# Performance work log

Measured on AMD Instinct MI355X. Metric: run time of the kernel, lower is better.

Reference implementation:

```python
import jax, jax.numpy as jnp
import numpy as np

KNN_K = 200
NUM_CLASSES = 400
TEMPERATURE = 0.07


def setup_inputs() -> dict:
    key = jax.random.key(0)
    k1, k2, k3 = jax.random.split(key, 3)
    q_knn = jax.random.normal(k1, (256, 128), dtype=jnp.float32)
    memory = jax.random.normal(k2, (500000, 128), dtype=jnp.float32)
    train_labels = jax.random.randint(k3, (500000,), 0, NUM_CLASSES, dtype=jnp.int64)
    return {"q_knn": q_knn, "memory": memory, "train_labels": train_labels}


def reference(q_knn, memory, train_labels):
    # dist: [N, M] similarity matmul (einsum 'nc,mc->nm')
    dist = jnp.einsum("nc,mc->nm", q_knn, memory)
    # top-k neighbors (sorted, largest)
    yd, yi = jax.lax.top_k(dist, KNN_K)          # [N, K], [N, K]
    retrieval = train_labels[yi]                  # [N, K] gathered labels
    # weighted one-hot vote: scatter-add exp(yd / T) into class bins
    w = jnp.exp(yd / TEMPERATURE)                 # [N, K]
    n = q_knn.shape[0]
    rows = jnp.arange(n)[:, None]                 # [N, 1] broadcast over K
    preds = jnp.zeros((n, NUM_CLASSES), dtype=q_knn.dtype).at[rows, retrieval].add(w)
    return preds
```

## Files before the change

### kernel.cpp

```cpp
#include <hip/hip_runtime.h>
#include <cfloat>
#include <math.h>


#define N_Q 256
#define KDIM 128
#define M_MEM 500000
#define NUM_CLASSES 400
#define KNN_K 200
#define INV_T (1.0f / 0.07f)
#define EXP_ARG_CLAMP 80.0f
#define Z_THR 3.0f

#define CAP_MAX 8192
#define PADB 136
#define M_TILE 64
#define T_PER 11
#define N_TILES64 7813
#define GEMM_GRID 711
#define BUF_CAP 1024

#define OFF_THR 0
#define OFF_CNT 1024
#define OFF_FLAG 2048
#define OFF_AFRAG 4096
#define OFF_CAND 69632

typedef __attribute__((ext_vector_type(8))) short short8;
typedef __attribute__((ext_vector_type(4))) float f32x4;

__device__ __forceinline__ unsigned short f2bf(float x) {
    unsigned u = __float_as_uint(x);
    return (unsigned short)((u + 0x7fffu + ((u >> 16) & 1u)) >> 16);
}

__global__ __launch_bounds__(256) void k_prep(const float* __restrict__ q,
                                              float* __restrict__ thr,
                                              int* __restrict__ cnt,
                                              int* __restrict__ flag,
                                              const int* __restrict__ lab32,
                                              short* __restrict__ afrag) {
    int tid = threadIdx.x;
    if (blockIdx.x == 0) {
        const float4* q4 = (const float4*)q;
        float s = 0.f;
#pragma unroll 8
        for (int i = 0; i < 32; i++) {
            float4 v = q4[tid * 32 + i];
            s = fmaf(v.x, v.x, s);
            s = fmaf(v.y, v.y, s);
            s = fmaf(v.z, v.z, s);
            s = fmaf(v.w, v.w, s);
        }
        thr[tid] = Z_THR * sqrtf(s);
        cnt[tid] = 0;
        __shared__ int s_any;
        if (tid == 0) s_any = 0;
        __syncthreads();
        int any = 0;
        for (int i = tid; i < 1024; i += 256) any |= lab32[2 * i + 1];
        if (any) atomicOr(&s_any, 1);
        __syncthreads();
        if (tid == 0) *flag = (s_any == 0) ? 1 : 0;
    } else {
        int e = (blockIdx.x - 1) * 256 + tid;
        int lane = e & 63, ks = (e >> 6) & 3, NT = e >> 8;
        int n = NT * 16 + (lane & 15);
        int k0 = ks * 32 + (lane >> 4) * 8;
        const float4* q4 = (const float4*)q;
        float4 a = q4[n * 32 + k0 / 4];
        float4 b = q4[n * 32 + k0 / 4 + 1];
        short8 o;
        o[0] = f2bf(a.x); o[1] = f2bf(a.y); o[2] = f2bf(a.z); o[3] = f2bf(a.w);
        o[4] = f2bf(b.x); o[5] = f2bf(b.y); o[6] = f2bf(b.z); o[7] = f2bf(b.w);
        ((short8*)afrag)[e] = o;
    }
}

#define PF_ISSUE(PF, TILE)                                                   \
    {                                                                        \
        int mb_ = m0 + (TILE) * M_TILE;                                      \
        _Pragma("unroll") for (int p = 0; p < 4; p++) {                      \
            int gm = mb_ + p * 16 + row0;                                    \
            if (gm >= M_MEM) gm = M_MEM - 1;                                 \
            int gi = gm * 32 + kg * 2;                                       \
            PF[p][0] = mem4[gi];                                             \
            PF[p][1] = mem4[gi + 1];                                         \
        }                                                                    \
    }

#define TILE_BODY(T, PF, BUFIDX)                                             \
    {                                                                        \
        short* B = Bs[BUFIDX];                                               \
        _Pragma("unroll") for (int p = 0; p < 4; p++) {                      \
            short8 o;                                                        \
            o[0] = f2bf(PF[p][0].x); o[1] = f2bf(PF[p][0].y);                \
            o[2] = f2bf(PF[p][0].z); o[3] = f2bf(PF[p][0].w);                \
            o[4] = f2bf(PF[p][1].x); o[5] = f2bf(PF[p][1].y);                \
            o[6] = f2bf(PF[p][1].z); o[7] = f2bf(PF[p][1].w);                \
            *(short8*)&B[(p * 16 + row0) * PADB + kg * 8] = o;               \
        }                                                                    \
        __syncthreads();                                                     \
        if ((T) + 2 < ntile) PF_ISSUE(PF, (T) + 2);                          \
        int mt0 = m0 + (T) * M_TILE;                                         \
        _Pragma("unroll") for (int mt = 0; mt < 4; mt++) {                   \
            int mrow = mt * 16 + ml;                                         \
            short8 bf[4];                                                    \
            _Pragma("unroll") for (int ks = 0; ks < 4; ks++)                 \
                bf[ks] = *(const short8*)&B[mrow * PADB + ks * 32 + quad * 8];\
            f32x4 acc[4];                                                    \
            _Pragma("unroll") for (int nt = 0; nt < 4; nt++)                 \
                acc[nt] = (f32x4){0.f, 0.f, 0.f, 0.f};                       \
            _Pragma("unroll") for (int nt = 0; nt < 4; nt++)                 \
                _Pragma("unroll") for (int ks = 0; ks < 4; ks++)             \
                    acc[nt] = __builtin_amdgcn_mfma_f32_16x16x32_bf16(       \
                        af[nt][ks], bf[ks], acc[nt], 0, 0, 0);               \
            int m = mt0 + mt * 16 + ml;                                      \
            bool mvalid = (m < M_MEM);                                       \
            _Pragma("unroll") for (int nt = 0; nt < 4; nt++) {               \
                bool any = (acc[nt][0] >= tr[nt][0]) |                       \
                           (acc[nt][1] >= tr[nt][1]) |                       \
                           (acc[nt][2] >= tr[nt][2]) |                       \
                           (acc[nt][3] >= tr[nt][3]);                        \
                if (mvalid & any) {                                          \
                    int nb = wn + nt * 16 + quad * 4;                        \
                    _Pragma("unroll") for (int r = 0; r < 4; r++) {          \
                        float v = acc[nt][r];                                \
                        if (v >= tr[nt][r]) {                                \
                            int p = atomicAdd(&s_nap, 1);                    \
                            if (p < BUF_CAP)                                 \
                                sbuf[p] = make_uint2(                        \
                                    __float_as_uint(v),                      \
                                    (unsigned)m | ((unsigned)(nb + r) << 19));\
                        }                                                    \
                    }                                                        \
                }                                                            \
            }                                                                \
        }                                                                    \
    }

__global__ __launch_bounds__(256) void k_gemm(const short* __restrict__ afrag,
                                              const float* __restrict__ mem,
                                              const float* __restrict__ thr,
                                              int* __restrict__ cnt,
                                              uint2* __restrict__ cand,
                                              int cap) {
    __shared__ short Bs[2][M_TILE * PADB];
    __shared__ uint2 sbuf[BUF_CAP];
    __shared__ int s_nap;
    int tid = threadIdx.x, lane = tid & 63, w = tid >> 6;
    int quad = lane >> 4, ml = lane & 15;
    int wn = w * 64;

    if (tid == 0) s_nap = 0;

    short8 af[4][4];
    const short8* afv = (const short8*)afrag;
#pragma unroll
    for (int nt = 0; nt < 4; nt++) {
        int NT = w * 4 + nt;
#pragma unroll
        for (int ks = 0; ks < 4; ks++) af[nt][ks] = afv[(NT * 4 + ks) * 64 + lane];
    }
    float tr[4][4];
#pragma unroll
    for (int nt = 0; nt < 4; nt++)
#pragma unroll
        for (int r = 0; r < 4; r++) tr[nt][r] = thr[wn + nt * 16 + quad * 4 + r];

    int t0 = blockIdx.x * T_PER;
    int ntile = N_TILES64 - t0;
    if (ntile > T_PER) ntile = T_PER;

    int row0 = tid >> 4, kg = tid & 15;
    const float4* mem4 = (const float4*)mem;
    int m0 = t0 * M_TILE;

    float4 pfA[4][2], pfB[4][2];
    if (ntile > 0) PF_ISSUE(pfA, 0);
    if (ntile > 1) PF_ISSUE(pfB, 1);

    for (int t = 0; t < ntile; t += 2) {
        TILE_BODY(t, pfA, 0);
        if (t + 1 < ntile) TILE_BODY(t + 1, pfB, 1);
    }

    __syncthreads();
    int total = s_nap;
    if (total > BUF_CAP) total = BUF_CAP;
    for (int i = tid; i < total; i += 256) {
        uint2 e = sbuf[i];
        int n = (int)(e.y >> 19);
        unsigned m = e.y & 0x7FFFFu;
        int pos = atomicAdd(&cnt[n], 1);
        if (pos < cap) cand[(long)n * cap + pos] = make_uint2(e.x, m);
    }
}

__global__ __launch_bounds__(256) void k_select(const uint2* __restrict__ cand,
                                                const int* __restrict__ cnt,
                                                const int* __restrict__ lab32,
                                                const int* __restrict__ flag,
                                                float* __restrict__ out, int cap) {
    __shared__ float sv[CAP_MAX];
    __shared__ float bins[NUM_CLASSES];
    int r = blockIdx.x, tid = threadIdx.x;
    int is64 = *flag;
    int cn = cnt[r];
    if (cn > cap) cn = cap;
    for (int i = tid; i < NUM_CLASSES; i += 256) bins[i] = 0.f;
    const uint2* cr = &cand[(long)r * cap];
    for (int i = tid; i < cn; i += 256) sv[i] = __uint_as_float(cr[i].x);
    __syncthreads();

    float v0 = -FLT_MAX, v1 = -FLT_MAX, v2 = -FLT_MAX, v3 = -FLT_MAX;
    if (tid < cn)       v0 = sv[tid];
    if (tid + 256 < cn) v1 = sv[tid + 256];
    if (tid + 512 < cn) v2 = sv[tid + 512];
    if (tid + 768 < cn) v3 = sv[tid + 768];
    int r0 = 0, r1 = 0, r2 = 0, r3 = 0;
    for (int i = 0; i < cn; i++) {
        float x = sv[i];
        r0 += (x > v0);
        r1 += (x > v1);
        r2 += (x > v2);
        r3 += (x > v3);
    }
#define VOTE(c, val, rk, valid)                                              \
    if ((valid) && (rk) < KNN_K) {                                           \
        int mm = (int)cr[c].y;                                               \
        int lab = is64 ? lab32[2 * mm] : lab32[mm];                          \
        if ((unsigned)lab < NUM_CLASSES) {                                   \
                \
            float wgt = expf(fminf((val) * INV_T, EXP_ARG_CLAMP));           \
            atomicAdd(&bins[lab], wgt);                                      \
        }                                                                    \
    }
    VOTE(tid, v0, r0, tid < cn)
    VOTE(tid + 256, v1, r1, tid + 256 < cn)
    VOTE(tid + 512, v2, r2, tid + 512 < cn)
    VOTE(tid + 768, v3, r3, tid + 768 < cn)
#undef VOTE
    __syncthreads();
    for (int c = tid; c < NUM_CLASSES; c += 256)
        out[r * NUM_CLASSES + c] = bins[c];
}

extern "C" void kernel_launch(void* const* d_in, const int* in_sizes, int n_in,
                              void* d_out, int out_size, void* d_ws, size_t ws_size,
                              hipStream_t stream) {
    const float* q = (const float*)d_in[0];
    const float* mem = (const float*)d_in[1];
    const int* lab = (const int*)d_in[2];
    float* out = (float*)d_out;

    char* ws = (char*)d_ws;
    float* thr = (float*)(ws + OFF_THR);
    int* cnt = (int*)(ws + OFF_CNT);
    int* flag = (int*)(ws + OFF_FLAG);
    short* afrag = (short*)(ws + OFF_AFRAG);
    uint2* cand = (uint2*)(ws + OFF_CAND);

    int cap = CAP_MAX;
    if (ws_size > OFF_CAND) {
        size_t maxcap = (ws_size - OFF_CAND) / (256ull * 8ull);
        if ((size_t)cap > maxcap) cap = (int)maxcap;
    }

    k_prep<<<17, 256, 0, stream>>>(q, thr, cnt, flag, lab, afrag);
    k_gemm<<<GEMM_GRID, 256, 0, stream>>>(afrag, mem, thr, cnt, cand, cap);
    k_select<<<256, 256, 0, stream>>>(cand, cnt, lab, flag, out, cap);
}
```

Baseline: 439.1 us.

## Restructure GEMM so each wave owns memory rows and streams all queries from LDS

Swaps the roles in the similarity GEMM. Query fragments and thresholds now sit in LDS, and each wave loads its own 16 memory rows straight from global memory into registers as the B operand, covering all 256 queries with 16 accumulator tiles. This drops the shared B staging buffer and the per-tile __syncthreads, and the grid becomes 512 blocks of 4 waves striding over 31250 row groups. In exchange every MFMA now reads its A operand from LDS, and holding 64 accumulator registers per thread may lower occupancy.

```diff
diff --git a/kernel.cpp b/kernel.cpp
--- a/kernel.cpp
+++ b/kernel.cpp
@@ -13,11 +13,9 @@
 #define Z_THR 3.0f
 
 #define CAP_MAX 8192
-#define PADB 136
-#define M_TILE 64
-#define T_PER 11
-#define N_TILES64 7813
-#define GEMM_GRID 711
+#define NBODY 31250
+#define NWAVES 2048
+#define GEMM_GRID 512
 #define BUF_CAP 1024
 
 #define OFF_THR 0
@@ -77,62 +75,54 @@
     }
 }
 
-#define PF_ISSUE(PF, TILE)                                                   \
+#define PF_ISSUE(BANK, S)                                                    \
     {                                                                        \
-        int mb_ = m0 + (TILE) * M_TILE;                                      \
-        _Pragma("unroll") for (int p = 0; p < 4; p++) {                      \
-            int gm = mb_ + p * 16 + row0;                                    \
-            if (gm >= M_MEM) gm = M_MEM - 1;                                 \
-            int gi = gm * 32 + kg * 2;                                       \
-            PF[p][0] = mem4[gi];                                             \
-            PF[p][1] = mem4[gi + 1];                                         \
-        }                                                                    \
-    }
-
-#define TILE_BODY(T, PF, BUFIDX)                                             \
+        int fi_ = ((g + (S) * NWAVES) * 16 + ml) * 32 + quad * 2;            \
+        _Pragma("unroll") for (int ks = 0; ks < 4; ks++) {                   \
+            BANK[ks * 2]     = mem4[fi_ + ks * 8];                           \
+            BANK[ks * 2 + 1] = mem4[fi_ + ks * 8 + 1];                       \
+        }                                                                    \
+    }
+
+#define BODY(S, BANK)                                                        \
     {                                                                        \
-        short* B = Bs[BUFIDX];                                               \
-        _Pragma("unroll") for (int p = 0; p < 4; p++) {                      \
+        short8 bf[4];                                                        \
+        _Pragma("unroll") for (int ks = 0; ks < 4; ks++) {                   \
             short8 o;                                                        \
-            o[0] = f2bf(PF[p][0].x); o[1] = f2bf(PF[p][0].y);                \
-            o[2] = f2bf(PF[p][0].z); o[3] = f2bf(PF[p][0].w);                \
-            o[4] = f2bf(PF[p][1].x); o[5] = f2bf(PF[p][1].y);                \
-            o[6] = f2bf(PF[p][1].z); o[7] = f2bf(PF[p][1].w);                \
-            *(short8*)&B[(p * 16 + row0) * PADB + kg * 8] = o;               \
-        }                                                                    \
-        __syncthreads();                                                     \
-        if ((T) + 2 < ntile) PF_ISSUE(PF, (T) + 2);                          \
-        int mt0 = m0 + (T) * M_TILE;                                         \
-        _Pragma("unroll") for (int mt = 0; mt < 4; mt++) {                   \
-            int mrow = mt * 16 + ml;                                         \
-            short8 bf[4];                                                    \
-            _Pragma("unroll") for (int ks = 0; ks < 4; ks++)                 \
-                bf[ks] = *(const short8*)&B[mrow * PADB + ks * 32 + quad * 8];\
-            f32x4 acc[4];                                                    \
-            _Pragma("unroll") for (int nt = 0; nt < 4; nt++)                 \
-                acc[nt] = (f32x4){0.f, 0.f, 0.f, 0.f};                       \
-            _Pragma("unroll") for (int nt = 0; nt < 4; nt++)                 \
-                _Pragma("unroll") for (int ks = 0; ks < 4; ks++)             \
-                    acc[nt] = __builtin_amdgcn_mfma_f32_16x16x32_bf16(       \
-                        af[nt][ks], bf[ks], acc[nt], 0, 0, 0);               \
-            int m = mt0 + mt * 16 + ml;                                      \
-            bool mvalid = (m < M_MEM);                                       \
-            _Pragma("unroll") for (int nt = 0; nt < 4; nt++) {               \
-                bool any = (acc[nt][0] >= tr[nt][0]) |                       \
-                           (acc[nt][1] >= tr[nt][1]) |                       \
-                           (acc[nt][2] >= tr[nt][2]) |                       \
-                           (acc[nt][3] >= tr[nt][3]);                        \
-                if (mvalid & any) {                                          \
-                    int nb = wn + nt * 16 + quad * 4;                        \
-                    _Pragma("unroll") for (int r = 0; r < 4; r++) {          \
-                        float v = acc[nt][r];                                \
-                        if (v >= tr[nt][r]) {                                \
-                            int p = atomicAdd(&s_nap, 1);                    \
-                            if (p < BUF_CAP)                                 \
-                                sbuf[p] = make_uint2(                        \
-                                    __float_as_uint(v),                      \
-                                    (unsigned)m | ((unsigned)(nb + r) << 19));\
-                        }                                                    \
+            o[0] = f2bf(BANK[ks * 2].x);     o[1] = f2bf(BANK[ks * 2].y);    \
+            o[2] = f2bf(BANK[ks * 2].z);     o[3] = f2bf(BANK[ks * 2].w);    \
+            o[4] = f2bf(BANK[ks * 2 + 1].x); o[5] = f2bf(BANK[ks * 2 + 1].y);\
+            o[6] = f2bf(BANK[ks * 2 + 1].z); o[7] = f2bf(BANK[ks * 2 + 1].w);\
+            bf[ks] = o;                                                      \
+        }                                                                    \
+        if ((S) + 2 < nb) PF_ISSUE(BANK, (S) + 2);                           \
+        f32x4 acc[16];                                                       \
+        _Pragma("unroll") for (int nt = 0; nt < 16; nt++)                    \
+            acc[nt] = (f32x4){0.f, 0.f, 0.f, 0.f};                           \
+        _Pragma("unroll") for (int nt = 0; nt < 16; nt++)                    \
+            _Pragma("unroll") for (int ks = 0; ks < 4; ks++) {               \
+                short8 a8 = af_lds[(nt * 4 + ks) * 64 + lane];               \
+                acc[nt] = __builtin_amdgcn_mfma_f32_16x16x32_bf16(           \
+                    a8, bf[ks], acc[nt], 0, 0, 0);                           \
+            }                                                                \
+        int m = (g + (S) * NWAVES) * 16 + ml;                                \
+        _Pragma("unroll") for (int nt = 0; nt < 16; nt++) {                  \
+            float4 tv = *(const float4*)&thr_lds[nt * 16 + quad * 4];        \
+            bool any = (acc[nt][0] >= tv.x) | (acc[nt][1] >= tv.y) |         \
+                       (acc[nt][2] >= tv.z) | (acc[nt][3] >= tv.w);          \
+            if (any) {                                                       \
+                int nb_ = nt * 16 + quad * 4;                                \
+                float tr0 = tv.x, tr1 = tv.y, tr2 = tv.z, tr3 = tv.w;        \
+                _Pragma("unroll") for (int r = 0; r < 4; r++) {              \
+                    float v = acc[nt][r];                                    \
+                    float trr = (r == 0) ? tr0 : (r == 1) ? tr1              \
+                              : (r == 2) ? tr2 : tr3;                        \
+                    if (v >= trr) {                                          \
+                        int p = atomicAdd(&s_nap, 1);                        \
+                        if (p < BUF_CAP)                                     \
+                            sbuf[p] = make_uint2(                            \
+                                __float_as_uint(v),                          \
+                                (unsigned)m | ((unsigned)(nb_ + r) << 19));  \
                     }                                                        \
                 }                                                            \
             }                                                                \
@@ -145,44 +135,31 @@
                                               int* __restrict__ cnt,
                                               uint2* __restrict__ cand,
                                               int cap) {
-    __shared__ short Bs[2][M_TILE * PADB];
+    __shared__ short8 af_lds[4096];
+    __shared__ float thr_lds[256];
     __shared__ uint2 sbuf[BUF_CAP];
     __shared__ int s_nap;
     int tid = threadIdx.x, lane = tid & 63, w = tid >> 6;
     int quad = lane >> 4, ml = lane & 15;
-    int wn = w * 64;
 
     if (tid == 0) s_nap = 0;
-
-    short8 af[4][4];
     const short8* afv = (const short8*)afrag;
 #pragma unroll
-    for (int nt = 0; nt < 4; nt++) {
-        int NT = w * 4 + nt;
-#pragma unroll
-        for (int ks = 0; ks < 4; ks++) af[nt][ks] = afv[(NT * 4 + ks) * 64 + lane];
-    }
-    float tr[4][4];
-#pragma unroll
-    for (int nt = 0; nt < 4; nt++)
-#pragma unroll
-        for (int r = 0; r < 4; r++) tr[nt][r] = thr[wn + nt * 16 + quad * 4 + r];
-
-    int t0 = blockIdx.x * T_PER;
-    int ntile = N_TILES64 - t0;
-    if (ntile > T_PER) ntile = T_PER;
-
-    int row0 = tid >> 4, kg = tid & 15;
+    for (int i = 0; i < 16; i++) af_lds[i * 256 + tid] = afv[i * 256 + tid];
+    thr_lds[tid] = thr[tid];
+    __syncthreads();
+
+    int g = blockIdx.x * 4 + w;
+    int nb = (NBODY + NWAVES - 1 - g) >> 11;
     const float4* mem4 = (const float4*)mem;
-    int m0 = t0 * M_TILE;
-
-    float4 pfA[4][2], pfB[4][2];
-    if (ntile > 0) PF_ISSUE(pfA, 0);
-    if (ntile > 1) PF_ISSUE(pfB, 1);
-
-    for (int t = 0; t < ntile; t += 2) {
-        TILE_BODY(t, pfA, 0);
-        if (t + 1 < ntile) TILE_BODY(t + 1, pfB, 1);
+
+    float4 pA[8], pB[8];
+    if (nb > 0) PF_ISSUE(pA, 0);
+    if (nb > 1) PF_ISSUE(pB, 1);
+
+    for (int s = 0; s < nb; s += 2) {
+        BODY(s, pA);
+        if (s + 1 < nb) BODY(s + 1, pB);
     }
 
     __syncthreads();
```

Measured after the change: 468.3 us. 1.07x slower.
